# Performance work log

Hardware: AMD Instinct MI355X
Metric: run time of the kernel (lower is better)

## Reference

```python
import jax, jax.numpy as jnp
import numpy as np

STOCH_LENGTH = 8  # default `length` in Stochify.forward


def setup_inputs() -> dict:
    key = jax.random.key(0)
    k1, k2 = jax.random.split(key)
    B, K, N = 4096, 2048, 2048
    x = jax.random.normal(k1, (B, K), dtype=jnp.float32)
    # weight init: normal(0, sqrt(2/(in+out))), shape [out, in]
    weight = jax.random.normal(k2, (N, K), dtype=jnp.float32) * np.sqrt(2.0 / (K + N))
    bias = jnp.zeros((N,), dtype=jnp.float32)
    return {"x": x, "weight": weight, "bias": bias}


def _to_stoch(key, v, length):
    """Bipolar stochastic bitstream encode: bit_l ~ Bernoulli((v+1)/2), shape [L, *v.shape]."""
    p = jnp.clip((v + 1.0) * 0.5, 0.0, 1.0)
    u = jax.random.uniform(key, (length,) + v.shape, dtype=v.dtype)
    return (u < p).astype(v.dtype)


def reference(x, weight, bias):
    # Stochify.forward: api = to_stoch(input, L); apw = to_stoch(weight.t(), L)
    # out = stoch.mm(api, apw, bipolar=True, output_stoch=False) + bias
    # Bipolar stochastic multiply is XNOR of bits; decoded product value per (i,j,k):
    #   2/L * sum_l XNOR(a,b) - 1.  Summed over k:
    #   out[i,j] = (2/L) * sum_{k,l} (2 a b - a - b + 1) - K
    # which reduces to per-slice matmuls plus row/col bit-count corrections
    # (avoids materializing the [B,K,N,L] XNOR tensor).
    L = STOCH_LENGTH
    K = x.shape[1]
    kA, kB = jax.random.split(jax.random.key(42))
    A = _to_stoch(kA, x, L)            # [L, B, K] bits in {0,1}
    Wb = _to_stoch(kB, weight.T, L)    # [L, K, N]
    S = jnp.einsum('lbk,lkn->bn', A, Wb)  # sum_{k,l} a*b
    sA = A.sum(axis=(0, 2))            # [B]  sum_{k,l} a
    sB = Wb.sum(axis=(0, 1))           # [N]  sum_{k,l} b
    xnor_count = 2.0 * S - sA[:, None] - sB[None, :] + K * L
    out = (2.0 / L) * xnor_count - K
    return out + bias[None, :]
```

## Files before the change

### kernel.cpp

```cpp
#include <hip/hip_runtime.h>
#include <stdint.h>


#define B_DIM 4096
#define K_DIM 2048
#define N_DIM 2048
#define WORDS 256

__host__ __device__ static inline void tf2x32(uint32_t ks0, uint32_t ks1,
                                              uint32_t x0, uint32_t x1,
                                              uint32_t* o0, uint32_t* o1) {
  uint32_t ks2 = ks0 ^ ks1 ^ 0x1BD11BDAu;
  x0 += ks0; x1 += ks1;
#define TF_RND(r) { x0 += x1; x1 = (x1 << (r)) | (x1 >> (32 - (r))); x1 ^= x0; }
  TF_RND(13) TF_RND(15) TF_RND(26) TF_RND(6)
  x0 += ks1; x1 += ks2 + 1u;
  TF_RND(17) TF_RND(29) TF_RND(16) TF_RND(24)
  x0 += ks2; x1 += ks0 + 2u;
  TF_RND(13) TF_RND(15) TF_RND(26) TF_RND(6)
  x0 += ks0; x1 += ks1 + 3u;
  TF_RND(17) TF_RND(29) TF_RND(16) TF_RND(24)
  x0 += ks1; x1 += ks2 + 4u;
  TF_RND(13) TF_RND(15) TF_RND(26) TF_RND(6)
  x0 += ks2; x1 += ks0 + 5u;
  *o0 = x0; *o1 = x1;
#undef TF_RND
}

__global__ __launch_bounds__(256) void stoch_bits_x(const float* __restrict__ x,
                                                    unsigned long long* __restrict__ Ap,
                                                    uint32_t k0, uint32_t k1) {
  unsigned gw = (unsigned)blockIdx.x * 4u + (threadIdx.x >> 6);
  unsigned lane = threadIdx.x & 63u;
  unsigned kw = gw & 31u;
  unsigned b  = (gw >> 5) & 4095u;
  unsigned l  = gw >> 17;
  unsigned k  = (kw << 6) + lane;
  uint32_t idx = ((l << 12) + b) * 2048u + k;
  uint32_t o0, o1;
  tf2x32(k0, k1, 0u, idx, &o0, &o1);
  uint32_t bits = o0 ^ o1;
  float u = __uint_as_float((bits >> 9) | 0x3F800000u) - 1.0f;
  float v = x[(size_t)b * 2048u + k];
  float p = fminf(fmaxf((v + 1.0f) * 0.5f, 0.0f), 1.0f);
  unsigned long long m = __ballot(u < p);
  if (lane == 0) Ap[(size_t)b * WORDS + (l << 5) + kw] = m;
}

__global__ __launch_bounds__(256) void stoch_bits_w(const float* __restrict__ wgt,
                                                    unsigned long long* __restrict__ Wp,
                                                    uint32_t k0, uint32_t k1) {
  unsigned gw = (unsigned)blockIdx.x * 4u + (threadIdx.x >> 6);
  unsigned lane = threadIdx.x & 63u;
  unsigned kw = gw & 31u;
  unsigned n  = (gw >> 5) & 2047u;
  unsigned l  = gw >> 16;
  unsigned k  = (kw << 6) + lane;
  uint32_t idx = ((l << 11) + k) * 2048u + n;
  uint32_t o0, o1;
  tf2x32(k0, k1, 0u, idx, &o0, &o1);
  uint32_t bits = o0 ^ o1;
  float u = __uint_as_float((bits >> 9) | 0x3F800000u) - 1.0f;
  float v = wgt[(size_t)n * 2048u + k];
  float p = fminf(fmaxf((v + 1.0f) * 0.5f, 0.0f), 1.0f);
  unsigned long long m = __ballot(u < p);
  if (lane == 0) Wp[(size_t)n * WORDS + (l << 5) + kw] = m;
}

__global__ __launch_bounds__(256) void xnor_gemm(const unsigned long long* __restrict__ Ap,
                                                 const unsigned long long* __restrict__ Wp,
                                                 const float* __restrict__ bias,
                                                 float* __restrict__ out) {
  __shared__ unsigned long long As[64][33];
  __shared__ unsigned long long Ws[64][33];
  const int tid = threadIdx.x;
  const int brow = blockIdx.y << 6;
  const int bcol = blockIdx.x << 6;
  const int tx = tid & 15, ty = tid >> 4;
  uint32_t cnt[4][4] = {};
#pragma unroll 1
  for (int c = 0; c < 8; ++c) {
    if (c) __syncthreads();
#pragma unroll
    for (int i = 0; i < 8; ++i) {
      int idx = tid + (i << 8);
      int r = idx >> 5, w = idx & 31;
      As[r][w] = Ap[(size_t)(brow + r) * WORDS + (c << 5) + w];
      Ws[r][w] = Wp[(size_t)(bcol + r) * WORDS + (c << 5) + w];
    }
    __syncthreads();
#pragma unroll 8
    for (int w = 0; w < 32; ++w) {
      unsigned long long av[4], bv[4];
#pragma unroll
      for (int i = 0; i < 4; ++i) av[i] = As[(ty << 2) + i][w];
#pragma unroll
      for (int j = 0; j < 4; ++j) bv[j] = Ws[(tx << 2) + j][w];
#pragma unroll
      for (int i = 0; i < 4; ++i)
#pragma unroll
        for (int j = 0; j < 4; ++j)
          cnt[i][j] += (uint32_t)__popcll(av[i] ^ bv[j]);
    }
  }
#pragma unroll
  for (int i = 0; i < 4; ++i) {
    int r = brow + (ty << 2) + i;
#pragma unroll
    for (int j = 0; j < 4; ++j) {
      int n = bcol + (tx << 2) + j;
      out[(size_t)r * N_DIM + n] = 2048.0f - 0.25f * (float)cnt[i][j] + bias[n];
    }
  }
}

extern "C" void kernel_launch(void* const* d_in, const int* in_sizes, int n_in,
                              void* d_out, int out_size, void* d_ws, size_t ws_size,
                              hipStream_t stream) {
  const float* x = (const float*)d_in[0];
  const float* wgt = (const float*)d_in[1];
  const float* bias = (const float*)d_in[2];
  float* out = (float*)d_out;

  unsigned long long* Ap = (unsigned long long*)d_ws;
  unsigned long long* Wp = Ap + (size_t)B_DIM * WORDS;

  uint32_t kA0, kA1, kB0, kB1;
  tf2x32(0u, 42u, 0u, 0u, &kA0, &kA1);
  tf2x32(0u, 42u, 0u, 1u, &kB0, &kB1);

  stoch_bits_x<<<262144, 256, 0, stream>>>(x, Ap, kA0, kA1);
  stoch_bits_w<<<131072, 256, 0, stream>>>(wgt, Wp, kB0, kB1);
  dim3 grid(N_DIM / 64, B_DIM / 64);
  xnor_gemm<<<grid, 256, 0, stream>>>(Ap, Wp, bias, out);
  (void)in_sizes; (void)n_in; (void)out_size; (void)ws_size;
}
```

Before: 567.9 us.

## Restructure bit generation per row and widen XNOR GEMM tile to 64x128

The bit-packing kernels now launch one block per row. Each thread loads its input value once and produces all 8 stream lengths in a loop, and the uniform comparison becomes an integer-to-float compare against a scaled threshold. The GEMM tile doubles in N to 128, with each thread holding 4x8 counters and reading strided columns to reduce shared-memory bank conflicts. This aims to cut redundant input loads and launch overhead and to raise arithmetic reuse per shared load, at the cost of more registers and lower occupancy.

```diff
diff --git a/kernel.cpp b/kernel.cpp
--- a/kernel.cpp
+++ b/kernel.cpp
@@ -6,6 +6,8 @@
 #define K_DIM 2048
 #define N_DIM 2048
 #define WORDS 256
+
+typedef unsigned long long u64;
 
 __host__ __device__ static inline void tf2x32(uint32_t ks0, uint32_t ks1,
                                               uint32_t x0, uint32_t x1,
@@ -28,56 +30,80 @@
 }
 
 __global__ __launch_bounds__(256) void stoch_bits_x(const float* __restrict__ x,
-                                                    unsigned long long* __restrict__ Ap,
+                                                    u64* __restrict__ Ap,
                                                     uint32_t k0, uint32_t k1) {
-  unsigned gw = (unsigned)blockIdx.x * 4u + (threadIdx.x >> 6);
-  unsigned lane = threadIdx.x & 63u;
-  unsigned kw = gw & 31u;
-  unsigned b  = (gw >> 5) & 4095u;
-  unsigned l  = gw >> 17;
-  unsigned k  = (kw << 6) + lane;
-  uint32_t idx = ((l << 12) + b) * 2048u + k;
-  uint32_t o0, o1;
-  tf2x32(k0, k1, 0u, idx, &o0, &o1);
-  uint32_t bits = o0 ^ o1;
-  float u = __uint_as_float((bits >> 9) | 0x3F800000u) - 1.0f;
-  float v = x[(size_t)b * 2048u + k];
-  float p = fminf(fmaxf((v + 1.0f) * 0.5f, 0.0f), 1.0f);
-  unsigned long long m = __ballot(u < p);
-  if (lane == 0) Ap[(size_t)b * WORDS + (l << 5) + kw] = m;
+  const unsigned b = blockIdx.x;
+  const unsigned lane = threadIdx.x & 63u;
+  const unsigned wv = threadIdx.x >> 6;
+  const float* xrow = x + (size_t)b * K_DIM;
+  u64* arow = Ap + (size_t)b * WORDS;
+#pragma unroll 1
+  for (int i = 0; i < 8; ++i) {
+    const unsigned kw = wv * 8u + (unsigned)i;
+    const unsigned k = (kw << 6) + lane;
+    const float v = xrow[k];
+    const float p = fminf(fmaxf((v + 1.0f) * 0.5f, 0.0f), 1.0f);
+    const float t = p * 8388608.0f;
+    const uint32_t base = b * 2048u + k;
+    u64 wbuf[8];
+#pragma unroll
+    for (int l = 0; l < 8; ++l) {
+      uint32_t idx = base + ((uint32_t)l << 23);
+      uint32_t o0, o1;
+      tf2x32(k0, k1, 0u, idx, &o0, &o1);
+      uint32_t m = (o0 ^ o1) >> 9;
+      wbuf[l] = __ballot((float)m < t);
+    }
+    if (lane == 0) {
+#pragma unroll
+      for (int l = 0; l < 8; ++l) arow[(l << 5) + kw] = wbuf[l];
+    }
+  }
 }
 
 __global__ __launch_bounds__(256) void stoch_bits_w(const float* __restrict__ wgt,
-                                                    unsigned long long* __restrict__ Wp,
+                                                    u64* __restrict__ Wp,
                                                     uint32_t k0, uint32_t k1) {
-  unsigned gw = (unsigned)blockIdx.x * 4u + (threadIdx.x >> 6);
-  unsigned lane = threadIdx.x & 63u;
-  unsigned kw = gw & 31u;
-  unsigned n  = (gw >> 5) & 2047u;
-  unsigned l  = gw >> 16;
-  unsigned k  = (kw << 6) + lane;
-  uint32_t idx = ((l << 11) + k) * 2048u + n;
-  uint32_t o0, o1;
-  tf2x32(k0, k1, 0u, idx, &o0, &o1);
-  uint32_t bits = o0 ^ o1;
-  float u = __uint_as_float((bits >> 9) | 0x3F800000u) - 1.0f;
-  float v = wgt[(size_t)n * 2048u + k];
-  float p = fminf(fmaxf((v + 1.0f) * 0.5f, 0.0f), 1.0f);
-  unsigned long long m = __ballot(u < p);
-  if (lane == 0) Wp[(size_t)n * WORDS + (l << 5) + kw] = m;
+  const unsigned n = blockIdx.x;
+  const unsigned lane = threadIdx.x & 63u;
+  const unsigned wv = threadIdx.x >> 6;
+  const float* wrow = wgt + (size_t)n * K_DIM;
+  u64* prow = Wp + (size_t)n * WORDS;
+#pragma unroll 1
+  for (int i = 0; i < 8; ++i) {
+    const unsigned kw = wv * 8u + (unsigned)i;
+    const unsigned k = (kw << 6) + lane;
+    const float v = wrow[k];
+    const float p = fminf(fmaxf((v + 1.0f) * 0.5f, 0.0f), 1.0f);
+    const float t = p * 8388608.0f;
+    const uint32_t base = k * 2048u + n;
+    u64 wbuf[8];
+#pragma unroll
+    for (int l = 0; l < 8; ++l) {
+      uint32_t idx = base + ((uint32_t)l << 22);
+      uint32_t o0, o1;
+      tf2x32(k0, k1, 0u, idx, &o0, &o1);
+      uint32_t m = (o0 ^ o1) >> 9;
+      wbuf[l] = __ballot((float)m < t);
+    }
+    if (lane == 0) {
+#pragma unroll
+      for (int l = 0; l < 8; ++l) prow[(l << 5) + kw] = wbuf[l];
+    }
+  }
 }
 
-__global__ __launch_bounds__(256) void xnor_gemm(const unsigned long long* __restrict__ Ap,
-                                                 const unsigned long long* __restrict__ Wp,
+__global__ __launch_bounds__(256) void xnor_gemm(const u64* __restrict__ Ap,
+                                                 const u64* __restrict__ Wp,
                                                  const float* __restrict__ bias,
                                                  float* __restrict__ out) {
-  __shared__ unsigned long long As[64][33];
-  __shared__ unsigned long long Ws[64][33];
+  __shared__ u64 As[64][33];
+  __shared__ u64 Ws[128][33];
   const int tid = threadIdx.x;
   const int brow = blockIdx.y << 6;
-  const int bcol = blockIdx.x << 6;
+  const int bcol = blockIdx.x << 7;
   const int tx = tid & 15, ty = tid >> 4;
-  uint32_t cnt[4][4] = {};
+  uint32_t cnt[4][8] = {};
 #pragma unroll 1
   for (int c = 0; c < 8; ++c) {
     if (c) __syncthreads();
@@ -86,20 +112,25 @@
       int idx = tid + (i << 8);
       int r = idx >> 5, w = idx & 31;
       As[r][w] = Ap[(size_t)(brow + r) * WORDS + (c << 5) + w];
+    }
+#pragma unroll
+    for (int i = 0; i < 16; ++i) {
+      int idx = tid + (i << 8);
+      int r = idx >> 5, w = idx & 31;
       Ws[r][w] = Wp[(size_t)(bcol + r) * WORDS + (c << 5) + w];
     }
     __syncthreads();
-#pragma unroll 8
+#pragma unroll 2
     for (int w = 0; w < 32; ++w) {
-      unsigned long long av[4], bv[4];
+      u64 av[4], bv[8];
 #pragma unroll
       for (int i = 0; i < 4; ++i) av[i] = As[(ty << 2) + i][w];
 #pragma unroll
-      for (int j = 0; j < 4; ++j) bv[j] = Ws[(tx << 2) + j][w];
+      for (int j = 0; j < 8; ++j) bv[j] = Ws[tx + (j << 4)][w];
 #pragma unroll
       for (int i = 0; i < 4; ++i)
 #pragma unroll
-        for (int j = 0; j < 4; ++j)
+        for (int j = 0; j < 8; ++j)
           cnt[i][j] += (uint32_t)__popcll(av[i] ^ bv[j]);
     }
   }
@@ -107,8 +138,8 @@
   for (int i = 0; i < 4; ++i) {
     int r = brow + (ty << 2) + i;
 #pragma unroll
-    for (int j = 0; j < 4; ++j) {
-      int n = bcol + (tx << 2) + j;
+    for (int j = 0; j < 8; ++j) {
+      int n = bcol + tx + (j << 4);
       out[(size_t)r * N_DIM + n] = 2048.0f - 0.25f * (float)cnt[i][j] + bias[n];
     }
   }
@@ -122,16 +153,16 @@
   const float* bias = (const float*)d_in[2];
   float* out = (float*)d_out;
 
-  unsigned long long* Ap = (unsigned long long*)d_ws;
-  unsigned long long* Wp = Ap + (size_t)B_DIM * WORDS;
+  u64* Ap = (u64*)d_ws;
+  u64* Wp = Ap + (size_t)B_DIM * WORDS;
 
   uint32_t kA0, kA1, kB0, kB1;
   tf2x32(0u, 42u, 0u, 0u, &kA0, &kA1);
   tf2x32(0u, 42u, 0u, 1u, &kB0, &kB1);
 
-  stoch_bits_x<<<262144, 256, 0, stream>>>(x, Ap, kA0, kA1);
-  stoch_bits_w<<<131072, 256, 0, stream>>>(wgt, Wp, kB0, kB1);
-  dim3 grid(N_DIM / 64, B_DIM / 64);
+  stoch_bits_x<<<B_DIM, 256, 0, stream>>>(x, Ap, kA0, kA1);
+  stoch_bits_w<<<N_DIM, 256, 0, stream>>>(wgt, Wp, kB0, kB1);
+  dim3 grid(N_DIM / 128, B_DIM / 64);
   xnor_gemm<<<grid, 256, 0, stream>>>(Ap, Wp, bias, out);
   (void)in_sizes; (void)n_in; (void)out_size; (void)ws_size;
 }
```

New measurement: 601.6 us. +5.9%, slower.
